# Performance work log

Hardware: AMD Instinct MI355X
Metric: run time of the kernel (lower is better)

The kernel has to match this reference:

```python
import jax, jax.numpy as jnp
import numpy as np
from jax import lax

N, D, H, E = 8192, 1024, 4096, 8


def setup_inputs() -> dict:
    key = jax.random.key(0)
    ks = jax.random.split(key, 4)
    return {
        "x": jax.random.normal(ks[0], (N, D), dtype=jnp.float32),
        "wg": jax.random.normal(ks[1], (D, E), dtype=jnp.float32) * 0.001,
        "fc1_w": jax.random.normal(ks[2], (E, D, H), dtype=jnp.float32) * 0.001,
        "fc1_b": jnp.zeros((E, 1, H), dtype=jnp.float32),
        "fc2_w": jax.random.normal(ks[3], (E, H, D), dtype=jnp.float32) * 0.001,
        "fc2_b": jnp.zeros((E, 1, D), dtype=jnp.float32),
        "k": 2,
    }


def reference(x, wg, fc1_w, fc1_b, fc2_w, fc2_b, k):
    n, d = x.shape
    e = wg.shape[1]
    cap = (k * n) // e  # expert capacity (capacity factor 1.0)

    # --- gate ---
    scores = jax.nn.softmax(x @ wg, axis=-1)          # [N,E]
    topv, topi = lax.top_k(scores, k)                 # [N,k]

    # --- top-k routing: position of each (token, slot) within its expert buffer ---
    masks = jax.nn.one_hot(topi, e, dtype=jnp.int32)  # [N,k,E]
    # slot-major priority: all slot-0 assignments before slot-1
    m = jnp.transpose(masks, (1, 0, 2)).reshape(k * n, e)
    pos_flat = jnp.cumsum(m, axis=0) - m              # position before own assignment
    pos = jnp.sum(pos_flat * m, axis=1).reshape(k, n).T   # [N,k]
    valid = pos < cap                                  # capacity overflow -> dropped

    # --- load-balance aux loss (top-1 fraction * mean gate prob) ---
    me = scores.mean(axis=0)                           # [E]
    ce = masks[:, 0, :].astype(scores.dtype).mean(axis=0)
    l_aux = e * jnp.sum(me * ce)

    # --- encode (dispatch): scatter tokens into [E, C, D] buffers ---
    w = valid.astype(x.dtype)                          # [N,k]
    flat_idx = topi * cap + jnp.where(valid, pos, 0)   # [N,k]
    contrib = (x[:, None, :] * w[:, :, None]).reshape(-1, d)
    dispatched = jnp.zeros((e * cap, d), x.dtype).at[flat_idx.reshape(-1)].add(contrib)
    dispatched = dispatched.reshape(e, cap, d)

    # --- batched expert FFN (all-to-all is identity on one device) ---
    h = jax.nn.relu(jnp.einsum('ecd,edh->ech', dispatched, fc1_w) + fc1_b)
    y = jnp.einsum('ech,ehd->ecd', h, fc2_w) + fc2_b   # [E,C,D]

    # --- decode (combine): gather back and weight by gate scores ---
    gathered = y.reshape(e * cap, d)[flat_idx]         # [N,k,D]
    output = jnp.einsum('nk,nkd->nd', topv * w, gathered)
    return output, l_aux
```

## Files before the change

### kernel.cpp

```cpp
#include <hip/hip_runtime.h>
#include <hip/hip_bf16.h>
#include <stdint.h>

#define N_TOK 8192
#define DMODEL 1024
#define HDIM 4096
#define NEXP 8
#define CAP 2048
#define GATE_BLOCKS (N_TOK / 4)

typedef float floatx4 __attribute__((ext_vector_type(4)));
typedef int int32x4_t __attribute__((ext_vector_type(4)));
typedef int int32x8_t __attribute__((ext_vector_type(8)));

static __device__ __forceinline__ void async_copy16(const void* g, void* l) {
  __builtin_amdgcn_global_load_lds(
      (const __attribute__((address_space(1))) void*)g,
      (__attribute__((address_space(3))) void*)l, 16, 0, 0);
}

static __device__ __forceinline__ unsigned int pk4_fp8(float a, float b, float c, float d) {
  int r = __builtin_amdgcn_cvt_pk_fp8_f32(a, b, 0, 0);
  r = __builtin_amdgcn_cvt_pk_fp8_f32(c, d, r, 1);
  return (unsigned int)r;
}

static __device__ __forceinline__ unsigned short f2bf(float f) {
  union { float f; uint32_t u; } v; v.f = f;
  uint32_t r = (v.u + 0x7FFFu + ((v.u >> 16) & 1u)) >> 16;
  return (unsigned short)r;
}

static __device__ __forceinline__ float bf2f(unsigned short u) {
  union { float f; uint32_t u32; } v; v.u32 = ((uint32_t)u) << 16;
  return v.f;
}

__global__ __launch_bounds__(256) void gate_kernel(
    const float* __restrict__ x, const float* __restrict__ wg,
    float* __restrict__ topv, int* __restrict__ topi,
    float* __restrict__ me_part, int* __restrict__ ce_part) {
  __shared__ float sm_p[4][NEXP];
  __shared__ int sm_i0[4];
  int wave = threadIdx.x >> 6;
  int lane = threadIdx.x & 63;
  int n = blockIdx.x * 4 + wave;
  float acc[NEXP];
#pragma unroll
  for (int e = 0; e < NEXP; e++) acc[e] = 0.f;
  const float* xr = x + (size_t)n * DMODEL;
#pragma unroll 4
  for (int i = 0; i < DMODEL / 64; i++) {
    int idx = lane + 64 * i;
    float xv = xr[idx];
    const float4* wr = (const float4*)(wg + (size_t)idx * NEXP);
    float4 w0 = wr[0], w1 = wr[1];
    acc[0] += xv * w0.x; acc[1] += xv * w0.y;
    acc[2] += xv * w0.z; acc[3] += xv * w0.w;
    acc[4] += xv * w1.x; acc[5] += xv * w1.y;
    acc[6] += xv * w1.z; acc[7] += xv * w1.w;
  }
#pragma unroll
  for (int e = 0; e < NEXP; e++) {
    float v = acc[e];
#pragma unroll
    for (int off = 32; off > 0; off >>= 1) v += __shfl_down(v, off, 64);
    acc[e] = v;
  }
  if (lane == 0) {
    float mx = acc[0];
#pragma unroll
    for (int e = 1; e < NEXP; e++) mx = fmaxf(mx, acc[e]);
    float p[NEXP]; float s = 0.f;
#pragma unroll
    for (int e = 0; e < NEXP; e++) { p[e] = expf(acc[e] - mx); s += p[e]; }
    float inv = 1.f / s;
#pragma unroll
    for (int e = 0; e < NEXP; e++) p[e] *= inv;
    int i0 = 0; float v0 = p[0];
#pragma unroll
    for (int e = 1; e < NEXP; e++) if (p[e] > v0) { v0 = p[e]; i0 = e; }
    int i1 = -1; float v1 = -1.f;
#pragma unroll
    for (int e = 0; e < NEXP; e++) {
      if (e == i0) continue;
      if (p[e] > v1) { v1 = p[e]; i1 = e; }
    }
    topv[n * 2] = v0; topv[n * 2 + 1] = v1;
    topi[n * 2] = i0; topi[n * 2 + 1] = i1;
#pragma unroll
    for (int e = 0; e < NEXP; e++) sm_p[wave][e] = p[e];
    sm_i0[wave] = i0;
  }
  __syncthreads();
  if (threadIdx.x < NEXP) {
    int e = threadIdx.x;
    float pm = 0.f; int cc = 0;
#pragma unroll
    for (int w = 0; w < 4; w++) {
      pm += sm_p[w][e];
      cc += (sm_i0[w] == e) ? 1 : 0;
    }
    me_part[blockIdx.x * NEXP + e] = pm;
    ce_part[blockIdx.x * NEXP + e] = cc;
  }
}

__global__ __launch_bounds__(1024) void scan_kernel(
    const int* __restrict__ topi, const float* __restrict__ topv,
    int* __restrict__ flat_idx, float* __restrict__ cw) {
  __shared__ int hist[16][NEXP];
  __shared__ int base[NEXP];
  int tid = threadIdx.x;
  int w = tid >> 6, lane = tid & 63;
  if (tid < NEXP) base[tid] = 0;
  int vals[16];
#pragma unroll
  for (int c = 0; c < 16; c++) {
    int j = c * 1024 + tid;
    vals[c] = topi[(size_t)(j & 8191) * 2 + (j >> 13)];
  }
  __syncthreads();
  for (int c = 0; c < 16; c++) {
    int j = c * 1024 + tid;
    int slot = j >> 13;
    int n = j & 8191;
    int e = vals[c];
    int rank = 0;
#pragma unroll
    for (int ee = 0; ee < NEXP; ee++) {
      unsigned long long m = __ballot(e == ee);
      if (e == ee) rank = __popcll(m & ((1ull << lane) - 1ull));
      if (lane == ee) hist[w][ee] = __popcll(m);
    }
    __syncthreads();
    if (tid < NEXP) {
      int run = base[tid];
#pragma unroll
      for (int ww = 0; ww < 16; ww++) {
        int t = hist[ww][tid];
        hist[ww][tid] = run;
        run += t;
      }
      base[tid] = run;
    }
    __syncthreads();
    int pos = hist[w][e] + rank;
    bool valid = pos < CAP;
    flat_idx[n * 2 + slot] = e * CAP + (valid ? pos : 0);
    cw[n * 2 + slot] = valid ? topv[n * 2 + slot] : 0.f;
    __syncthreads();
  }
}

__global__ __launch_bounds__(256) void transpose_cvt_fp8(
    const float* __restrict__ in, unsigned char* __restrict__ out,
    int R, int C) {
  __shared__ float tile[32][129];
  const float* inp = in + (size_t)blockIdx.z * R * C;
  unsigned char* outp = out + (size_t)blockIdx.z * R * C;
  int c0 = blockIdx.x * 32, r0 = blockIdx.y * 128;
  int t = threadIdx.x;
#pragma unroll
  for (int p = 0; p < 4; p++) {
    int r = p * 32 + (t >> 3);
    int c4 = (t & 7) * 4;
    float4 v = *(const float4*)(inp + (size_t)(r0 + r) * C + c0 + c4);
    tile[c4 + 0][r] = v.x; tile[c4 + 1][r] = v.y;
    tile[c4 + 2][r] = v.z; tile[c4 + 3][r] = v.w;
  }
  __syncthreads();
  int c = t >> 3, r16 = (t & 7) * 16;
  unsigned int w[4];
#pragma unroll
  for (int j = 0; j < 4; j++) {
    float a = tile[c][r16 + j * 4 + 0] * 512.f;
    float b = tile[c][r16 + j * 4 + 1] * 512.f;
    float cc2 = tile[c][r16 + j * 4 + 2] * 512.f;
    float d = tile[c][r16 + j * 4 + 3] * 512.f;
    w[j] = pk4_fp8(a, b, cc2, d);
  }
  uint4 o; o.x = w[0]; o.y = w[1]; o.z = w[2]; o.w = w[3];
  *(uint4*)(outp + (size_t)(c0 + c) * R + r0 + r16) = o;
}

__global__ __launch_bounds__(64) void dispatch_kernel(
    const float* __restrict__ x, const int* __restrict__ flat_idx,
    const float* __restrict__ cw, unsigned char* __restrict__ disp) {
  int a = blockIdx.x;
  if (cw[a] == 0.f) return;
  int n = a >> 1;
  int f = flat_idx[a];
  int lane = threadIdx.x;
  const float4* xr = (const float4*)(x + (size_t)n * DMODEL);
  unsigned int* dr = (unsigned int*)(disp + (size_t)f * DMODEL);
#pragma unroll
  for (int i = 0; i < 4; i++) {
    float4 v = xr[lane + 64 * i];
    dr[lane + 64 * i] = pk4_fp8(v.x, v.y, v.z, v.w);
  }
}

template <int K_DIM, bool RELU, int OUT_MODE>
__global__ __launch_bounds__(256) void gemm_fp8_kernel(
    const unsigned char* __restrict__ A, const unsigned char* __restrict__ BT,
    const float* __restrict__ bias, void* __restrict__ Cout, int M, int Ncols,
    float inv_scale, float out_mult) {
  constexpr int BK = 128;
  constexpr int NSTAGE = K_DIM / BK;
  static_assert(NSTAGE >= 2, "need >=2 K stages for the 2-deep pipeline");
  __shared__ unsigned char As[2][128 * BK];
  __shared__ unsigned char Bs[2][128 * BK];
  int e = blockIdx.z;
  int tn = blockIdx.x, tm = blockIdx.y;
  const unsigned char* Ae = A + (size_t)e * M * K_DIM + (size_t)tm * 128 * K_DIM;
  const unsigned char* Be = BT + (size_t)e * Ncols * K_DIM + (size_t)tn * 128 * K_DIM;
  int wv = threadIdx.x >> 6, l = threadIdx.x & 63;
  int wm = wv >> 1, wn = wv & 1;
  int l15 = l & 15, quad = l >> 4;
  int rbase = wv * 8 + (l >> 3);
  int cg = (l & 7) ^ ((l >> 3) & 7);
  floatx4 acc[4][4] = {};

#define STAGE_LOADS(k0, buf)                                                   \
  {                                                                            \
    _Pragma("unroll") for (int i = 0; i < 4; i++) {                            \
      int r = rbase + i * 32;                                                  \
      async_copy16(Ae + (size_t)r * K_DIM + (k0) + cg * 16,                    \
                   &As[buf][i * 4096 + wv * 1024]);                            \
      async_copy16(Be + (size_t)r * K_DIM + (k0) + cg * 16,                    \
                   &Bs[buf][i * 4096 + wv * 1024]);                            \
    }                                                                          \
  }

  STAGE_LOADS(0, 0);
  STAGE_LOADS(BK, 1);
#pragma unroll
  for (int s = 0; s < NSTAGE; s++) {
    const int cur = s & 1;
    if (s + 1 < NSTAGE)
      asm volatile("s_waitcnt vmcnt(8)" ::: "memory");
    else
      asm volatile("s_waitcnt vmcnt(0)" ::: "memory");
    __builtin_amdgcn_s_barrier();
    int32x8_t af[4], bf[4];
#pragma unroll
    for (int mi = 0; mi < 4; mi++) {
      int m = wm * 64 + mi * 16 + l15;
      int x0 = (quad * 2) ^ (m & 7), x1 = (quad * 2 + 1) ^ (m & 7);
      int32x4_t lo = *(const int32x4_t*)(&As[cur][m * 128 + x0 * 16]);
      int32x4_t hi = *(const int32x4_t*)(&As[cur][m * 128 + x1 * 16]);
      af[mi] = __builtin_shufflevector(lo, hi, 0, 1, 2, 3, 4, 5, 6, 7);
    }
#pragma unroll
    for (int ni = 0; ni < 4; ni++) {
      int m = wn * 64 + ni * 16 + l15;
      int x0 = (quad * 2) ^ (m & 7), x1 = (quad * 2 + 1) ^ (m & 7);
      int32x4_t lo = *(const int32x4_t*)(&Bs[cur][m * 128 + x0 * 16]);
      int32x4_t hi = *(const int32x4_t*)(&Bs[cur][m * 128 + x1 * 16]);
      bf[ni] = __builtin_shufflevector(lo, hi, 0, 1, 2, 3, 4, 5, 6, 7);
    }
    asm volatile("s_waitcnt lgkmcnt(0)" ::: "memory");
    __builtin_amdgcn_s_barrier();
    if (s + 2 < NSTAGE) STAGE_LOADS((s + 2) * BK, cur);
    __builtin_amdgcn_s_setprio(1);
#pragma unroll
    for (int mi = 0; mi < 4; mi++)
#pragma unroll
      for (int ni = 0; ni < 4; ni++)
        acc[mi][ni] = __builtin_amdgcn_mfma_scale_f32_16x16x128_f8f6f4(
            af[mi], bf[ni], acc[mi][ni], 0, 0, 0, 0x7F7F7F7F, 0, 0x7F7F7F7F);
    __builtin_amdgcn_s_setprio(0);
  }
#undef STAGE_LOADS

  int row_base = tm * 128 + wm * 64;
  int col_base = tn * 128 + wn * 64;
  const float* be = bias + (size_t)e * Ncols;
#pragma unroll
  for (int ni = 0; ni < 4; ni++) {
    int col = col_base + ni * 16 + l15;
    float bv = be[col];
#pragma unroll
    for (int mi = 0; mi < 4; mi++) {
#pragma unroll
      for (int r = 0; r < 4; r++) {
        int row = row_base + mi * 16 + quad * 4 + r;
        float v = acc[mi][ni][r] * inv_scale + bv;
        if (RELU) v = fmaxf(v, 0.f);
        size_t idx = (size_t)e * M * Ncols + (size_t)row * Ncols + col;
        if (OUT_MODE == 1) {
          float s = fminf(fmaxf(v * out_mult, -440.f), 440.f);
          unsigned int b8 = (unsigned int)__builtin_amdgcn_cvt_pk_fp8_f32(s, s, 0, 0) & 0xFF;
          ((unsigned char*)Cout)[idx] = (unsigned char)b8;
        } else if (OUT_MODE == 2) {
          ((unsigned short*)Cout)[idx] = f2bf(v);
        } else {
          ((float*)Cout)[idx] = v;
        }
      }
    }
  }
}

__global__ __launch_bounds__(256) void combine_kernel(
    const unsigned short* __restrict__ y, const int* __restrict__ flat_idx,
    const float* __restrict__ cw, float* __restrict__ out) {
  int n = blockIdx.x;
  float w0 = cw[n * 2], w1 = cw[n * 2 + 1];
  int f0 = flat_idx[n * 2], f1 = flat_idx[n * 2 + 1];
  const ushort2* y0 = (const ushort2*)(y + (size_t)f0 * DMODEL);
  const ushort2* y1 = (const ushort2*)(y + (size_t)f1 * DMODEL);
  float2* o = (float2*)(out + (size_t)n * DMODEL);
  int t = threadIdx.x;
#pragma unroll
  for (int i = 0; i < 2; i++) {
    int j = t + i * 256;
    ushort2 a = y0[j], b = y1[j];
    float2 r;
    r.x = w0 * bf2f(a.x) + w1 * bf2f(b.x);
    r.y = w0 * bf2f(a.y) + w1 * bf2f(b.y);
    o[j] = r;
  }
}

__global__ __launch_bounds__(256) void laux_kernel(
    const float* __restrict__ me_part, const int* __restrict__ ce_part,
    float* __restrict__ out_laux) {
  __shared__ float sme[NEXP][33];
  __shared__ float sce[NEXP][33];
  int tid = threadIdx.x;
  int e = tid >> 5;
  int c = tid & 31;
  float pm = 0.f, cc = 0.f;
  for (int b = c; b < GATE_BLOCKS; b += 32) {
    pm += me_part[b * NEXP + e];
    cc += (float)ce_part[b * NEXP + e];
  }
  sme[e][c] = pm;
  sce[e][c] = cc;
  __syncthreads();
  if (tid < NEXP) {
    float tm = 0.f, tc = 0.f;
#pragma unroll
    for (int i = 0; i < 32; i++) { tm += sme[tid][i]; tc += sce[tid][i]; }
    sme[tid][32] = tm;
    sce[tid][32] = tc;
  }
  __syncthreads();
  if (tid == 0) {
    float s = 0.f;
#pragma unroll
    for (int ee = 0; ee < NEXP; ee++)
      s += (sme[ee][32] / (float)N_TOK) * (sce[ee][32] / (float)N_TOK);
    *out_laux = (float)NEXP * s;
  }
}

extern "C" void kernel_launch(void* const* d_in, const int* in_sizes, int n_in,
                              void* d_out, int out_size, void* d_ws,
                              size_t ws_size, hipStream_t stream) {
  (void)in_sizes; (void)n_in; (void)out_size; (void)ws_size;
  const float* x     = (const float*)d_in[0];
  const float* wg    = (const float*)d_in[1];
  const float* fc1_w = (const float*)d_in[2];
  const float* fc1_b = (const float*)d_in[3];
  const float* fc2_w = (const float*)d_in[4];
  const float* fc2_b = (const float*)d_in[5];
  float* out = (float*)d_out;

  char* ws = (char*)d_ws;
  size_t o = 0;
  unsigned char* fc1t = (unsigned char*)(ws + o); o += (size_t)NEXP * DMODEL * HDIM;
  unsigned char* fc2t = (unsigned char*)(ws + o); o += (size_t)NEXP * DMODEL * HDIM;
  unsigned char* disp = (unsigned char*)(ws + o); o += (size_t)NEXP * CAP * DMODEL;
  unsigned char* hbuf = (unsigned char*)(ws + o); o += (size_t)NEXP * CAP * HDIM;
  unsigned short* ybuf = (unsigned short*)(ws + o); o += (size_t)NEXP * CAP * DMODEL * 2;
  float* topv = (float*)(ws + o); o += (size_t)N_TOK * 2 * 4;
  int* topi   = (int*)(ws + o);   o += (size_t)N_TOK * 2 * 4;
  int* flat   = (int*)(ws + o);   o += (size_t)N_TOK * 2 * 4;
  float* cw   = (float*)(ws + o); o += (size_t)N_TOK * 2 * 4;
  float* mep  = (float*)(ws + o); o += (size_t)GATE_BLOCKS * NEXP * 4;
  int* cep    = (int*)(ws + o);   o += (size_t)GATE_BLOCKS * NEXP * 4;


  gate_kernel<<<GATE_BLOCKS, 256, 0, stream>>>(x, wg, topv, topi, mep, cep);
  scan_kernel<<<1, 1024, 0, stream>>>(topi, topv, flat, cw);
  transpose_cvt_fp8<<<dim3(HDIM / 32, DMODEL / 128, NEXP), 256, 0, stream>>>(fc1_w, fc1t, DMODEL, HDIM);
  transpose_cvt_fp8<<<dim3(DMODEL / 32, HDIM / 128, NEXP), 256, 0, stream>>>(fc2_w, fc2t, HDIM, DMODEL);
  dispatch_kernel<<<N_TOK * 2, 64, 0, stream>>>(x, flat, cw, disp);
  gemm_fp8_kernel<DMODEL, true, 1>
      <<<dim3(HDIM / 128, CAP / 128, NEXP), 256, 0, stream>>>(
          disp, fc1t, fc1_b, hbuf, CAP, HDIM, 1.f / 512.f, 16.f);
  gemm_fp8_kernel<HDIM, false, 2>
      <<<dim3(DMODEL / 128, CAP / 128, NEXP), 256, 0, stream>>>(
          hbuf, fc2t, fc2_b, ybuf, CAP, DMODEL, 1.f / 8192.f, 1.f);
  combine_kernel<<<N_TOK, 256, 0, stream>>>(ybuf, flat, cw, out);
  laux_kernel<<<1, 256, 0, stream>>>(mep, cep, out + (size_t)N_TOK * DMODEL);
}
```

Baseline: 588.9 us.

## Remap GEMM workgroups across XCDs and interleave LDS reads with MFMAs

Blocks of the FP8 expert GEMM get a remapped linear id, so consecutive tiles (sharing A/B panels) land on the same XCD chiplet and reuse its L2. The K-loop now issues all LDS fragment reads up front, then runs MFMAs for each A row-block as soon as its fragment arrives, using graded lgkmcnt waits and sched_barriers. Only the last row-block's MFMAs stay after the barrier and next-stage prefetch. The aim is to hide LDS latency behind matrix math and improve cache locality, at the cost of more brittle hand scheduling and a rigid barrier layout.

New measurement: 570.5 us. -3.1%, faster.

```diff
diff --git a/kernel.cpp b/kernel.cpp
--- a/kernel.cpp
+++ b/kernel.cpp
@@ -211,8 +211,23 @@
   static_assert(NSTAGE >= 2, "need >=2 K stages for the 2-deep pipeline");
   __shared__ unsigned char As[2][128 * BK];
   __shared__ unsigned char Bs[2][128 * BK];
-  int e = blockIdx.z;
-  int tn = blockIdx.x, tm = blockIdx.y;
+
+  unsigned gx = gridDim.x;
+  unsigned gxy = gridDim.x * gridDim.y;
+  unsigned nwg = gxy * gridDim.z;
+  unsigned lid = blockIdx.z * gxy + blockIdx.y * gx + blockIdx.x;
+  int e, tm, tn;
+  if ((nwg & 7u) == 0u) {
+    unsigned chunk = nwg >> 3;
+    unsigned w = (lid & 7u) * chunk + (lid >> 3);
+    e = w / gxy;
+    unsigned rem = w - (unsigned)e * gxy;
+    tm = rem / gx;
+    tn = rem - (unsigned)tm * gx;
+  } else {
+    e = blockIdx.z; tm = blockIdx.y; tn = blockIdx.x;
+  }
+
   const unsigned char* Ae = A + (size_t)e * M * K_DIM + (size_t)tm * 128 * K_DIM;
   const unsigned char* Be = BT + (size_t)e * Ncols * K_DIM + (size_t)tn * 128 * K_DIM;
   int wv = threadIdx.x >> 6, l = threadIdx.x & 63;
@@ -233,6 +248,15 @@
     }                                                                          \
   }
 
+#define READ_AF(mi)                                                            \
+  {                                                                            \
+    int m = wm * 64 + (mi) * 16 + l15;                                         \
+    int x0 = (quad * 2) ^ (m & 7), x1 = (quad * 2 + 1) ^ (m & 7);              \
+    int32x4_t lo = *(const int32x4_t*)(&As[cur][m * 128 + x0 * 16]);           \
+    int32x4_t hi = *(const int32x4_t*)(&As[cur][m * 128 + x1 * 16]);           \
+    af[mi] = __builtin_shufflevector(lo, hi, 0, 1, 2, 3, 4, 5, 6, 7);          \
+  }
+
   STAGE_LOADS(0, 0);
   STAGE_LOADS(BK, 1);
 #pragma unroll
@@ -245,14 +269,6 @@
     __builtin_amdgcn_s_barrier();
     int32x8_t af[4], bf[4];
 #pragma unroll
-    for (int mi = 0; mi < 4; mi++) {
-      int m = wm * 64 + mi * 16 + l15;
-      int x0 = (quad * 2) ^ (m & 7), x1 = (quad * 2 + 1) ^ (m & 7);
-      int32x4_t lo = *(const int32x4_t*)(&As[cur][m * 128 + x0 * 16]);
-      int32x4_t hi = *(const int32x4_t*)(&As[cur][m * 128 + x1 * 16]);
-      af[mi] = __builtin_shufflevector(lo, hi, 0, 1, 2, 3, 4, 5, 6, 7);
-    }
-#pragma unroll
     for (int ni = 0; ni < 4; ni++) {
       int m = wn * 64 + ni * 16 + l15;
       int x0 = (quad * 2) ^ (m & 7), x1 = (quad * 2 + 1) ^ (m & 7);
@@ -260,19 +276,45 @@
       int32x4_t hi = *(const int32x4_t*)(&Bs[cur][m * 128 + x1 * 16]);
       bf[ni] = __builtin_shufflevector(lo, hi, 0, 1, 2, 3, 4, 5, 6, 7);
     }
+    READ_AF(0);
+    __builtin_amdgcn_sched_barrier(0);
+    READ_AF(1);
+    READ_AF(2);
+    READ_AF(3);
+    __builtin_amdgcn_sched_barrier(0);
+    __builtin_amdgcn_s_setprio(1);
+    asm volatile("s_waitcnt lgkmcnt(6)" ::: "memory");
+    __builtin_amdgcn_sched_barrier(0);
+#pragma unroll
+    for (int ni = 0; ni < 4; ni++)
+      acc[0][ni] = __builtin_amdgcn_mfma_scale_f32_16x16x128_f8f6f4(
+          af[0], bf[ni], acc[0][ni], 0, 0, 0, 0x7F7F7F7F, 0, 0x7F7F7F7F);
+    asm volatile("s_waitcnt lgkmcnt(4)" ::: "memory");
+    __builtin_amdgcn_sched_barrier(0);
+#pragma unroll
+    for (int ni = 0; ni < 4; ni++)
+      acc[1][ni] = __builtin_amdgcn_mfma_scale_f32_16x16x128_f8f6f4(
+          af[1], bf[ni], acc[1][ni], 0, 0, 0, 0x7F7F7F7F, 0, 0x7F7F7F7F);
+    asm volatile("s_waitcnt lgkmcnt(2)" ::: "memory");
+    __builtin_amdgcn_sched_barrier(0);
+#pragma unroll
+    for (int ni = 0; ni < 4; ni++)
+      acc[2][ni] = __builtin_amdgcn_mfma_scale_f32_16x16x128_f8f6f4(
+          af[2], bf[ni], acc[2][ni], 0, 0, 0, 0x7F7F7F7F, 0, 0x7F7F7F7F);
     asm volatile("s_waitcnt lgkmcnt(0)" ::: "memory");
+    __builtin_amdgcn_sched_barrier(0);
+    __builtin_amdgcn_s_setprio(0);
     __builtin_amdgcn_s_barrier();
     if (s + 2 < NSTAGE) STAGE_LOADS((s + 2) * BK, cur);
     __builtin_amdgcn_s_setprio(1);
 #pragma unroll
-    for (int mi = 0; mi < 4; mi++)
-#pragma unroll
-      for (int ni = 0; ni < 4; ni++)
-        acc[mi][ni] = __builtin_amdgcn_mfma_scale_f32_16x16x128_f8f6f4(
-            af[mi], bf[ni], acc[mi][ni], 0, 0, 0, 0x7F7F7F7F, 0, 0x7F7F7F7F);
+    for (int ni = 0; ni < 4; ni++)
+      acc[3][ni] = __builtin_amdgcn_mfma_scale_f32_16x16x128_f8f6f4(
+          af[3], bf[ni], acc[3][ni], 0, 0, 0, 0x7F7F7F7F, 0, 0x7F7F7F7F);
     __builtin_amdgcn_s_setprio(0);
   }
 #undef STAGE_LOADS
+#undef READ_AF
 
   int row_base = tm * 128 + wm * 64;
   int col_base = tn * 128 + wn * 64;
```

## Enlarge FP8 GEMM tiles to 256x256 with 8 waves and interleave LDS reads with MFMAs

Applied to the files above, without the earlier changes.

Both expert GEMMs move from 128x128 tiles with 4 waves to 256x256 tiles with 8 waves. Each wave now computes a 128x64 sub-tile, which raises operand reuse and halves global traffic per output element. The A-fragment LDS reads are split into two halves and interleaved with MFMA rows using fine-grained lgkmcnt waits and sched_barriers, so LDS latency overlaps with compute. The trade-offs are 128KB of LDS per block, more accumulator registers, and far fewer blocks, which can hurt occupancy and load balance (fc2 gets only 256 blocks).

After: 581.7 us. About the same (-1.2%).

```diff
diff --git a/kernel.cpp b/kernel.cpp
--- a/kernel.cpp
+++ b/kernel.cpp
@@ -202,36 +202,59 @@
 }
 
 template <int K_DIM, bool RELU, int OUT_MODE>
-__global__ __launch_bounds__(256) void gemm_fp8_kernel(
+__global__ __launch_bounds__(512) void gemm_fp8_kernel(
     const unsigned char* __restrict__ A, const unsigned char* __restrict__ BT,
     const float* __restrict__ bias, void* __restrict__ Cout, int M, int Ncols,
     float inv_scale, float out_mult) {
   constexpr int BK = 128;
   constexpr int NSTAGE = K_DIM / BK;
   static_assert(NSTAGE >= 2, "need >=2 K stages for the 2-deep pipeline");
-  __shared__ unsigned char As[2][128 * BK];
-  __shared__ unsigned char Bs[2][128 * BK];
-  int e = blockIdx.z;
-  int tn = blockIdx.x, tm = blockIdx.y;
-  const unsigned char* Ae = A + (size_t)e * M * K_DIM + (size_t)tm * 128 * K_DIM;
-  const unsigned char* Be = BT + (size_t)e * Ncols * K_DIM + (size_t)tn * 128 * K_DIM;
+  __shared__ unsigned char As[2][256 * BK];
+  __shared__ unsigned char Bs[2][256 * BK];
+
+  int e = blockIdx.z, tm = blockIdx.y, tn = blockIdx.x;
+  const unsigned char* Ae = A + (size_t)e * M * K_DIM + (size_t)tm * 256 * K_DIM;
+  const unsigned char* Be = BT + (size_t)e * Ncols * K_DIM + (size_t)tn * 256 * K_DIM;
   int wv = threadIdx.x >> 6, l = threadIdx.x & 63;
-  int wm = wv >> 1, wn = wv & 1;
+  int wm = wv >> 2, wn = wv & 3;
   int l15 = l & 15, quad = l >> 4;
   int rbase = wv * 8 + (l >> 3);
   int cg = (l & 7) ^ ((l >> 3) & 7);
-  floatx4 acc[4][4] = {};
+  floatx4 acc[8][4] = {};
 
 #define STAGE_LOADS(k0, buf)                                                   \
   {                                                                            \
     _Pragma("unroll") for (int i = 0; i < 4; i++) {                            \
-      int r = rbase + i * 32;                                                  \
+      int r = rbase + i * 64;                                                  \
       async_copy16(Ae + (size_t)r * K_DIM + (k0) + cg * 16,                    \
-                   &As[buf][i * 4096 + wv * 1024]);                            \
+                   &As[buf][i * 8192 + wv * 1024]);                            \
       async_copy16(Be + (size_t)r * K_DIM + (k0) + cg * 16,                    \
-                   &Bs[buf][i * 4096 + wv * 1024]);                            \
+                   &Bs[buf][i * 8192 + wv * 1024]);                            \
     }                                                                          \
   }
+
+#define READ_BF(ni)                                                            \
+  {                                                                            \
+    int m = wn * 64 + (ni) * 16 + l15;                                         \
+    int x0 = (quad * 2) ^ (m & 7), x1 = (quad * 2 + 1) ^ (m & 7);              \
+    int32x4_t lo = *(const int32x4_t*)(&Bs[cur][m * 128 + x0 * 16]);           \
+    int32x4_t hi = *(const int32x4_t*)(&Bs[cur][m * 128 + x1 * 16]);           \
+    bf[ni] = __builtin_shufflevector(lo, hi, 0, 1, 2, 3, 4, 5, 6, 7);          \
+  }
+
+#define READ_AF(dst, mi)                                                       \
+  {                                                                            \
+    int m = wm * 128 + (mi) * 16 + l15;                                        \
+    int x0 = (quad * 2) ^ (m & 7), x1 = (quad * 2 + 1) ^ (m & 7);              \
+    int32x4_t lo = *(const int32x4_t*)(&As[cur][m * 128 + x0 * 16]);           \
+    int32x4_t hi = *(const int32x4_t*)(&As[cur][m * 128 + x1 * 16]);           \
+    (dst) = __builtin_shufflevector(lo, hi, 0, 1, 2, 3, 4, 5, 6, 7);           \
+  }
+
+#define MFMA_ROW(asrc, mi)                                                     \
+  _Pragma("unroll") for (int ni = 0; ni < 4; ni++)                             \
+      acc[mi][ni] = __builtin_amdgcn_mfma_scale_f32_16x16x128_f8f6f4(          \
+          (asrc), bf[ni], acc[mi][ni], 0, 0, 0, 0x7F7F7F7F, 0, 0x7F7F7F7F);
 
   STAGE_LOADS(0, 0);
   STAGE_LOADS(BK, 1);
@@ -243,46 +266,71 @@
     else
       asm volatile("s_waitcnt vmcnt(0)" ::: "memory");
     __builtin_amdgcn_s_barrier();
-    int32x8_t af[4], bf[4];
-#pragma unroll
-    for (int mi = 0; mi < 4; mi++) {
-      int m = wm * 64 + mi * 16 + l15;
-      int x0 = (quad * 2) ^ (m & 7), x1 = (quad * 2 + 1) ^ (m & 7);
-      int32x4_t lo = *(const int32x4_t*)(&As[cur][m * 128 + x0 * 16]);
-      int32x4_t hi = *(const int32x4_t*)(&As[cur][m * 128 + x1 * 16]);
-      af[mi] = __builtin_shufflevector(lo, hi, 0, 1, 2, 3, 4, 5, 6, 7);
-    }
-#pragma unroll
-    for (int ni = 0; ni < 4; ni++) {
-      int m = wn * 64 + ni * 16 + l15;
-      int x0 = (quad * 2) ^ (m & 7), x1 = (quad * 2 + 1) ^ (m & 7);
-      int32x4_t lo = *(const int32x4_t*)(&Bs[cur][m * 128 + x0 * 16]);
-      int32x4_t hi = *(const int32x4_t*)(&Bs[cur][m * 128 + x1 * 16]);
-      bf[ni] = __builtin_shufflevector(lo, hi, 0, 1, 2, 3, 4, 5, 6, 7);
-    }
+    int32x8_t afA[4], afB[4], bf[4];
+    READ_BF(0); READ_BF(1); READ_BF(2); READ_BF(3);
+    READ_AF(afA[0], 0);
+    __builtin_amdgcn_sched_barrier(0);
+    READ_AF(afA[1], 1);
+    __builtin_amdgcn_sched_barrier(0);
+    READ_AF(afA[2], 2);
+    __builtin_amdgcn_sched_barrier(0);
+    READ_AF(afA[3], 3);
+    __builtin_amdgcn_sched_barrier(0);
+    __builtin_amdgcn_s_setprio(1);
+    asm volatile("s_waitcnt lgkmcnt(6)" ::: "memory");
+    __builtin_amdgcn_sched_barrier(0);
+    MFMA_ROW(afA[0], 0);
+    asm volatile("s_waitcnt lgkmcnt(4)" ::: "memory");
+    __builtin_amdgcn_sched_barrier(0);
+    MFMA_ROW(afA[1], 1);
+    asm volatile("s_waitcnt lgkmcnt(2)" ::: "memory");
+    __builtin_amdgcn_sched_barrier(0);
+    MFMA_ROW(afA[2], 2);
     asm volatile("s_waitcnt lgkmcnt(0)" ::: "memory");
+    __builtin_amdgcn_sched_barrier(0);
+    MFMA_ROW(afA[3], 3);
+    __builtin_amdgcn_s_setprio(0);
+    READ_AF(afB[0], 4);
+    __builtin_amdgcn_sched_barrier(0);
+    READ_AF(afB[1], 5);
+    __builtin_amdgcn_sched_barrier(0);
+    READ_AF(afB[2], 6);
+    __builtin_amdgcn_sched_barrier(0);
+    READ_AF(afB[3], 7);
+    __builtin_amdgcn_sched_barrier(0);
+    __builtin_amdgcn_s_setprio(1);
+    asm volatile("s_waitcnt lgkmcnt(6)" ::: "memory");
+    __builtin_amdgcn_sched_barrier(0);
+    MFMA_ROW(afB[0], 4);
+    asm volatile("s_waitcnt lgkmcnt(4)" ::: "memory");
+    __builtin_amdgcn_sched_barrier(0);
+    MFMA_ROW(afB[1], 5);
+    asm volatile("s_waitcnt lgkmcnt(2)" ::: "memory");
+    __builtin_amdgcn_sched_barrier(0);
+    MFMA_ROW(afB[2], 6);
+    asm volatile("s_waitcnt lgkmcnt(0)" ::: "memory");
+    __builtin_amdgcn_sched_barrier(0);
+    __builtin_amdgcn_s_setprio(0);
     __builtin_amdgcn_s_barrier();
     if (s + 2 < NSTAGE) STAGE_LOADS((s + 2) * BK, cur);
     __builtin_amdgcn_s_setprio(1);
-#pragma unroll
-    for (int mi = 0; mi < 4; mi++)
-#pragma unroll
-      for (int ni = 0; ni < 4; ni++)
-        acc[mi][ni] = __builtin_amdgcn_mfma_scale_f32_16x16x128_f8f6f4(
-            af[mi], bf[ni], acc[mi][ni], 0, 0, 0, 0x7F7F7F7F, 0, 0x7F7F7F7F);
+    MFMA_ROW(afB[3], 7);
     __builtin_amdgcn_s_setprio(0);
   }
 #undef STAGE_LOADS
-
-  int row_base = tm * 128 + wm * 64;
-  int col_base = tn * 128 + wn * 64;
+#undef READ_BF
+#undef READ_AF
+#undef MFMA_ROW
+
+  int row_base = tm * 256 + wm * 128;
+  int col_base = tn * 256 + wn * 64;
   const float* be = bias + (size_t)e * Ncols;
 #pragma unroll
   for (int ni = 0; ni < 4; ni++) {
     int col = col_base + ni * 16 + l15;
     float bv = be[col];
 #pragma unroll
-    for (int mi = 0; mi < 4; mi++) {
+    for (int mi = 0; mi < 8; mi++) {
 #pragma unroll
       for (int r = 0; r < 4; r++) {
         int row = row_base + mi * 16 + quad * 4 + r;
@@ -390,10 +438,10 @@
   transpose_cvt_fp8<<<dim3(DMODEL / 32, HDIM / 128, NEXP), 256, 0, stream>>>(fc2_w, fc2t, HDIM, DMODEL);
   dispatch_kernel<<<N_TOK * 2, 64, 0, stream>>>(x, flat, cw, disp);
   gemm_fp8_kernel<DMODEL, true, 1>
-      <<<dim3(HDIM / 128, CAP / 128, NEXP), 256, 0, stream>>>(
+      <<<dim3(HDIM / 256, CAP / 256, NEXP), 512, 0, stream>>>(
           disp, fc1t, fc1_b, hbuf, CAP, HDIM, 1.f / 512.f, 16.f);
   gemm_fp8_kernel<HDIM, false, 2>
-      <<<dim3(DMODEL / 128, CAP / 128, NEXP), 256, 0, stream>>>(
+      <<<dim3(DMODEL / 256, CAP / 256, NEXP), 512, 0, stream>>>(
           hbuf, fc2t, fc2_b, ybuf, CAP, DMODEL, 1.f / 8192.f, 1.f);
   combine_kernel<<<N_TOK, 256, 0, stream>>>(ybuf, flat, cw, out);
   laux_kernel<<<1, 256, 0, stream>>>(mep, cep, out + (size_t)N_TOK * DMODEL);
```
